# Performance work log

Measured on AMD Instinct MI355X. Metric: run time of the kernel, lower is better.

## Reference

```python
import jax, jax.numpy as jnp
import numpy as np

QMIN, QMAX = -128, 127  # 8-bit signed quantized range


def setup_inputs() -> dict:
    key = jax.random.key(0)
    k0, k1, k2, k3 = jax.random.split(key, 4)
    N, Cin, H, W = 64, 128, 56, 56
    Cout, K = 128, 3
    x = jax.random.randint(k0, (N, Cin, H, W), -128, 128, dtype=jnp.int32).astype(jnp.int8)
    weight = jax.random.randint(k1, (Cout, Cin, K, K), -128, 128, dtype=jnp.int32).astype(jnp.int8)
    # int32 bias (already shifted by -Zx*sum(W) in the original quantization flow)
    bias = jax.random.randint(k2, (Cout,), -4096, 4096, dtype=jnp.int32)
    input_scale = jnp.float32(0.02)
    weight_scale = jax.random.uniform(k3, (Cout,), minval=0.001, maxval=0.01, dtype=jnp.float32)  # per-channel
    output_scale = jnp.float32(0.05)
    input_zero_point = -3   # python int, constant
    output_zero_point = -2  # python int, constant
    return {"x": x, "weight": weight, "bias": bias,
            "input_scale": input_scale, "weight_scale": weight_scale,
            "output_scale": output_scale,
            "input_zero_point": input_zero_point,
            "output_zero_point": output_zero_point}


def reference(x, weight, bias, input_scale, weight_scale, output_scale,
              input_zero_point, output_zero_point):
    # pad spatial dims with the INPUT zero point (padding=(1,1), as in the torch module)
    xp = jnp.pad(x, ((0, 0), (0, 0), (1, 1), (1, 1)), constant_values=input_zero_point)
    acc = jax.lax.conv_general_dilated(
        xp.astype(jnp.int32), weight.astype(jnp.int32),
        window_strides=(1, 1), padding='VALID',
        rhs_dilation=(1, 1), dimension_numbers=('NCHW', 'OIHW', 'NCHW'))
    acc = acc + bias[None, :, None, None]                       # [N,Co,Ho,Wo] int32
    # requantize: per-output-channel scale, shift by output zero point
    scale = (input_scale * weight_scale / output_scale)[None, :, None, None]
    out = acc.astype(jnp.float32) * scale + jnp.float32(output_zero_point)
    return jnp.clip(jnp.round(out), QMIN, QMAX).astype(jnp.int8)
```

## Files before the change

kernel.cpp:

```cpp
#include <hip/hip_runtime.h>


#define CIN  128
#define COUT 128
#define HW   56
#define NPIX (HW * HW)
#define ROWS  4
#define QCOLS 58
#define XROW  (QCOLS * CIN)
#define XP_OFF 147456
#define XP_ROWS (64 * QCOLS)
#define STEPS 36

typedef int v4i  __attribute__((ext_vector_type(4)));
typedef int v16i __attribute__((ext_vector_type(16)));

__device__ __forceinline__ void gl16(const void* g, void* l) {
    __builtin_amdgcn_global_load_lds(
        (const __attribute__((address_space(1))) unsigned*)g,
        (__attribute__((address_space(3))) unsigned*)l, 16, 0, 0);
}

__global__ __launch_bounds__(256) void pack_w2(const int* __restrict__ w_g,
                                               unsigned* __restrict__ wp2) {
    int i = blockIdx.x * 256 + threadIdx.x;
    if (i >= 36 * 128 * 8) return;
    int dw   = i & 7;
    int cout = (i >> 3) & 127;
    int step = i >> 10;
    int t  = step >> 2;
    int cb = step & 3;
    unsigned d = 0;
#pragma unroll
    for (int b = 0; b < 4; ++b) {
        int ci = cb * 32 + dw * 4 + b;
        int v = w_g[(cout * CIN + ci) * 9 + t];
        d |= (unsigned)(v & 0xFF) << (8 * b);
    }
    int g  = (cout << 1) | (dw >> 2);
    int gs = g ^ ((g >> 3) & 7);
    wp2[step * 1024 + gs * 4 + (dw & 3)] = d;
}

#define LSTR 57
__global__ __launch_bounds__(256) void repack_x(const int* __restrict__ x_g,
                                                unsigned char* __restrict__ xp,
                                                const int* __restrict__ zp_in_p) {
    __shared__ int lx[CIN * LSTR];
    const int blk = blockIdx.x;
    const int n  = blk / QCOLS;
    const int hp = blk % QCOLS;
    const int tid = threadIdx.x;
    const unsigned zpd = (unsigned)((*zp_in_p) & 0xFF) * 0x01010101u;
    unsigned* row = (unsigned*)(xp + (size_t)blk * XROW);

    if (hp == 0 || hp == QCOLS - 1) {
#pragma unroll
        for (int it = 0; it < 8; ++it) {
            int d = it * 256 + tid;
            if (d < QCOLS * 32) row[d] = zpd;
        }
        return;
    }
    const int h = hp - 1;
    const int* xrow = x_g + (n * CIN * HW + h) * HW;
#pragma unroll
    for (int it = 0; it < 7; ++it) {
        int idx = it * 256 + tid;
        int ci  = idx / 14;
        int w4  = (idx - ci * 14) * 4;
        v4i L = *(const v4i*)(xrow + ci * NPIX + w4);
        int* ld = &lx[ci * LSTR + w4];
        ld[0] = L[0]; ld[1] = L[1]; ld[2] = L[2]; ld[3] = L[3];
    }
    __syncthreads();
#pragma unroll
    for (int it = 0; it < 8; ++it) {
        int d = it * 256 + tid;
        if (d < QCOLS * 32) {
            int wp  = d >> 5;
            int ci4 = d & 31;
            unsigned v = zpd;
            if (wp >= 1 && wp <= HW) {
                const int* lb = &lx[ci4 * 4 * LSTR + (wp - 1)];
                v = (unsigned)(lb[0] & 0xFF) |
                    ((unsigned)(lb[LSTR] & 0xFF) << 8) |
                    ((unsigned)(lb[2 * LSTR] & 0xFF) << 16) |
                    ((unsigned)(lb[3 * LSTR] & 0xFF) << 24);
            }
            row[d] = v;
        }
    }
}

__global__ __launch_bounds__(256, 2) void conv_mfma(
    const unsigned char* __restrict__ xp, const unsigned char* __restrict__ wp2b,
    const int* __restrict__ bias, const float* __restrict__ in_s,
    const float* __restrict__ w_s, const float* __restrict__ out_s,
    const int* __restrict__ zp_out_p, int* __restrict__ out) {
    __shared__ unsigned char xsb[45056];
    __shared__ float scs[COUT];
    __shared__ int   bis[COUT];

    const int n   = blockIdx.x / 14;
    const int ho0 = (blockIdx.x % 14) * ROWS;
    const int tid    = threadIdx.x;
    const int lane   = tid & 63;
    const int wave   = tid >> 6;
    const int lane31 = lane & 31;
    const int hi     = lane >> 5;
    const int hi4    = hi * 4;

    if (tid < COUT) {
        scs[tid] = ((*in_s) / (*out_s)) * w_s[tid];
        bis[tid] = bias[tid];
    }

    const unsigned char* win = xp + (size_t)(n * QCOLS + ho0) * XROW;
    const int qrel = lane >> 3;
    const int lof  = (qrel * 8 + ((lane & 7) ^ qrel)) * 16;
    for (int i = wave; i < 44; i += 4) {
        int off = i * 1024 + lof;
        if (i == 43 && qrel >= 4) off = 0;
        gl16(win + off, xsb + i * 1024);
    }
    __syncthreads();

    const unsigned* xs = (const unsigned*)xsb;
    int qb0, qb1;
    {
        int px0 = wave * 64 + lane31;
        int px1 = wave * 64 + 32 + lane31;
        if (px1 > ROWS * HW - 1) px1 = ROWS * HW - 1;
        qb0 = (px0 / HW) * QCOLS + (px0 % HW);
        qb1 = (px1 / HW) * QCOLS + (px1 % HW);
    }
    const unsigned char *bpA, *bpB, *bpC, *bpD;
    {
        int g0 = 0 * 64 + lane31 * 2 + hi;
        int g1 = 1 * 64 + lane31 * 2 + hi;
        int g2 = 2 * 64 + lane31 * 2 + hi;
        int g3 = 3 * 64 + lane31 * 2 + hi;
        bpA = wp2b + (g0 ^ ((g0 >> 3) & 7)) * 16;
        bpB = wp2b + (g1 ^ ((g1 >> 3) & 7)) * 16;
        bpC = wp2b + (g2 ^ ((g2 >> 3) & 7)) * 16;
        bpD = wp2b + (g3 ^ ((g3 >> 3) & 7)) * 16;
    }

    v16i acc[2][4];
#pragma unroll
    for (int i = 0; i < 2; ++i)
#pragma unroll
        for (int j = 0; j < 4; ++j) acc[i][j] = (v16i)0;

    v4i c0[4], c1[4], c2[4];
#define LOADB(DST, S)                                                        \
    {                                                                        \
        DST[0] = *(const v4i*)(bpA + (S) * 4096);                            \
        DST[1] = *(const v4i*)(bpB + (S) * 4096);                            \
        DST[2] = *(const v4i*)(bpC + (S) * 4096);                            \
        DST[3] = *(const v4i*)(bpD + (S) * 4096);                            \
    }
#define BODY(S, CUR, NX2)                                                    \
    {                                                                        \
        if ((S) + 2 < STEPS) LOADB(NX2, (S) + 2);                            \
        const int t2 = (S) >> 2, cb = (S) & 3;                               \
        const int kr = (t2 * 11) >> 5;                                       \
        const int dq = kr * QCOLS + (t2 - 3 * kr);                           \
        const int q0 = qb0 + dq, q1 = qb1 + dq;                              \
        v4i a0 = *(const v4i*)&xs[q0 * 32 + ((cb * 8 + hi4) ^ ((q0 & 7) << 2))]; \
        v4i a1 = *(const v4i*)&xs[q1 * 32 + ((cb * 8 + hi4) ^ ((q1 & 7) << 2))]; \
        acc[0][0] = __builtin_amdgcn_mfma_i32_32x32x32_i8(CUR[0], a0, acc[0][0], 0, 0, 0); \
        acc[0][1] = __builtin_amdgcn_mfma_i32_32x32x32_i8(CUR[1], a0, acc[0][1], 0, 0, 0); \
        acc[0][2] = __builtin_amdgcn_mfma_i32_32x32x32_i8(CUR[2], a0, acc[0][2], 0, 0, 0); \
        acc[0][3] = __builtin_amdgcn_mfma_i32_32x32x32_i8(CUR[3], a0, acc[0][3], 0, 0, 0); \
        acc[1][0] = __builtin_amdgcn_mfma_i32_32x32x32_i8(CUR[0], a1, acc[1][0], 0, 0, 0); \
        acc[1][1] = __builtin_amdgcn_mfma_i32_32x32x32_i8(CUR[1], a1, acc[1][1], 0, 0, 0); \
        acc[1][2] = __builtin_amdgcn_mfma_i32_32x32x32_i8(CUR[2], a1, acc[1][2], 0, 0, 0); \
        acc[1][3] = __builtin_amdgcn_mfma_i32_32x32x32_i8(CUR[3], a1, acc[1][3], 0, 0, 0); \
    }

    LOADB(c0, 0);
    LOADB(c1, 1);
#pragma unroll 1
    for (int uu = 0; uu < 12; ++uu) {
        const int s = uu * 3;
        BODY(s + 0, c0, c2);
        BODY(s + 1, c1, c0);
        BODY(s + 2, c2, c1);
    }
#undef BODY
#undef LOADB

    const float zpo = (float)(*zp_out_p);
#pragma unroll
    for (int i = 0; i < 2; ++i) {
        const int px = wave * 64 + i * 32 + lane31;
        if (px < ROWS * HW) {
            int* ob = out + n * COUT * NPIX + ho0 * HW + px;
#pragma unroll
            for (int nt = 0; nt < 4; ++nt) {
#pragma unroll
                for (int reg = 0; reg < 16; ++reg) {
                    int co = nt * 32 + (reg & 3) + 8 * (reg >> 2) + hi4;
                    float f = fmaf((float)(acc[i][nt][reg] + bis[co]), scs[co], zpo);
                    f = rintf(f);
                    f = fminf(fmaxf(f, -128.0f), 127.0f);
                    ob[co * NPIX] = (int)f;
                }
            }
        }
    }
}

extern "C" void kernel_launch(void* const* d_in, const int* in_sizes, int n_in,
                              void* d_out, int out_size, void* d_ws, size_t ws_size,
                              hipStream_t stream) {
    const int* x_g      = (const int*)d_in[0];
    const int* w_g      = (const int*)d_in[1];
    const int* bias     = (const int*)d_in[2];
    const float* in_s   = (const float*)d_in[3];
    const float* w_s    = (const float*)d_in[4];
    const float* out_s  = (const float*)d_in[5];
    const int* zp_in_p  = (const int*)d_in[6];
    const int* zp_out_p = (const int*)d_in[7];
    int* outp = (int*)d_out;
    unsigned* wp2 = (unsigned*)d_ws;
    unsigned char* xpp = (unsigned char*)d_ws + XP_OFF;

    pack_w2<<<(36 * 128 * 8 + 255) / 256, 256, 0, stream>>>(w_g, wp2);
    repack_x<<<XP_ROWS, 256, 0, stream>>>(x_g, xpp, zp_in_p);

    const int nblocks = 64 * (HW / ROWS);
    conv_mfma<<<nblocks, 256, 0, stream>>>(xpp, (const unsigned char*)wp2, bias,
                                           in_s, w_s, out_s, zp_out_p, outp);
}
```

Before: 86.74 us.

## Stage weight tiles through LDS with a 4-deep async global_load_lds pipeline

```diff
diff --git a/kernel.cpp b/kernel.cpp
--- a/kernel.cpp
+++ b/kernel.cpp
@@ -10,7 +10,6 @@
 #define XROW  (QCOLS * CIN)
 #define XP_OFF 147456
 #define XP_ROWS (64 * QCOLS)
-#define STEPS 36
 
 typedef int v4i  __attribute__((ext_vector_type(4)));
 typedef int v16i __attribute__((ext_vector_type(16)));
@@ -99,6 +98,7 @@
     const float* __restrict__ w_s, const float* __restrict__ out_s,
     const int* __restrict__ zp_out_p, int* __restrict__ out) {
     __shared__ unsigned char xsb[45056];
+    __shared__ unsigned char Bb[4][8192];
     __shared__ float scs[COUT];
     __shared__ int   bis[COUT];
 
@@ -116,6 +116,15 @@
         bis[tid] = bias[tid];
     }
 
+#define STAGEB(U)                                                             \
+    {                                                                         \
+        const unsigned char* bs = wp2b + (U) * 8192 + wave * 2048 + lane * 16;\
+        unsigned char* bd = &Bb[(U) & 3][wave * 2048];                        \
+        gl16(bs, bd);                                                         \
+        gl16(bs + 1024, bd + 1024);                                           \
+    }
+
+    STAGEB(0); STAGEB(1); STAGEB(2);
     const unsigned char* win = xp + (size_t)(n * QCOLS + ho0) * XROW;
     const int qrel = lane >> 3;
     const int lof  = (qrel * 8 + ((lane & 7) ^ qrel)) * 16;
@@ -135,16 +144,11 @@
         qb0 = (px0 / HW) * QCOLS + (px0 % HW);
         qb1 = (px1 / HW) * QCOLS + (px1 % HW);
     }
-    const unsigned char *bpA, *bpB, *bpC, *bpD;
-    {
-        int g0 = 0 * 64 + lane31 * 2 + hi;
-        int g1 = 1 * 64 + lane31 * 2 + hi;
-        int g2 = 2 * 64 + lane31 * 2 + hi;
-        int g3 = 3 * 64 + lane31 * 2 + hi;
-        bpA = wp2b + (g0 ^ ((g0 >> 3) & 7)) * 16;
-        bpB = wp2b + (g1 ^ ((g1 >> 3) & 7)) * 16;
-        bpC = wp2b + (g2 ^ ((g2 >> 3) & 7)) * 16;
-        bpD = wp2b + (g3 ^ ((g3 >> 3) & 7)) * 16;
+    int boff[4];
+#pragma unroll
+    for (int nt = 0; nt < 4; ++nt) {
+        int g = nt * 64 + lane31 * 2 + hi;
+        boff[nt] = (g ^ ((g >> 3) & 7)) * 16;
     }
 
     v16i acc[2][4];
@@ -153,44 +157,60 @@
 #pragma unroll
         for (int j = 0; j < 4; ++j) acc[i][j] = (v16i)0;
 
-    v4i c0[4], c1[4], c2[4];
-#define LOADB(DST, S)                                                        \
-    {                                                                        \
-        DST[0] = *(const v4i*)(bpA + (S) * 4096);                            \
-        DST[1] = *(const v4i*)(bpB + (S) * 4096);                            \
-        DST[2] = *(const v4i*)(bpC + (S) * 4096);                            \
-        DST[3] = *(const v4i*)(bpD + (S) * 4096);                            \
-    }
-#define BODY(S, CUR, NX2)                                                    \
-    {                                                                        \
-        if ((S) + 2 < STEPS) LOADB(NX2, (S) + 2);                            \
-        const int t2 = (S) >> 2, cb = (S) & 3;                               \
-        const int kr = (t2 * 11) >> 5;                                       \
-        const int dq = kr * QCOLS + (t2 - 3 * kr);                           \
-        const int q0 = qb0 + dq, q1 = qb1 + dq;                              \
-        v4i a0 = *(const v4i*)&xs[q0 * 32 + ((cb * 8 + hi4) ^ ((q0 & 7) << 2))]; \
-        v4i a1 = *(const v4i*)&xs[q1 * 32 + ((cb * 8 + hi4) ^ ((q1 & 7) << 2))]; \
-        acc[0][0] = __builtin_amdgcn_mfma_i32_32x32x32_i8(CUR[0], a0, acc[0][0], 0, 0, 0); \
-        acc[0][1] = __builtin_amdgcn_mfma_i32_32x32x32_i8(CUR[1], a0, acc[0][1], 0, 0, 0); \
-        acc[0][2] = __builtin_amdgcn_mfma_i32_32x32x32_i8(CUR[2], a0, acc[0][2], 0, 0, 0); \
-        acc[0][3] = __builtin_amdgcn_mfma_i32_32x32x32_i8(CUR[3], a0, acc[0][3], 0, 0, 0); \
-        acc[1][0] = __builtin_amdgcn_mfma_i32_32x32x32_i8(CUR[0], a1, acc[1][0], 0, 0, 0); \
-        acc[1][1] = __builtin_amdgcn_mfma_i32_32x32x32_i8(CUR[1], a1, acc[1][1], 0, 0, 0); \
-        acc[1][2] = __builtin_amdgcn_mfma_i32_32x32x32_i8(CUR[2], a1, acc[1][2], 0, 0, 0); \
-        acc[1][3] = __builtin_amdgcn_mfma_i32_32x32x32_i8(CUR[3], a1, acc[1][3], 0, 0, 0); \
-    }
-
-    LOADB(c0, 0);
-    LOADB(c1, 1);
+#define COMPUTE(U)                                                            \
+    {                                                                         \
+        const int t  = (U) >> 1;                                              \
+        const int kr = (t * 11) >> 5;                                         \
+        const int dq = kr * QCOLS + (t - 3 * kr);                             \
+        const int q0 = qb0 + dq, q1 = qb1 + dq;                               \
+        const int s0 = (q0 & 7) << 2, s1 = (q1 & 7) << 2;                     \
+        const unsigned char* bb = Bb[(U) & 3];                                \
+        __builtin_amdgcn_s_setprio(1);                                        \
+        _Pragma("unroll")                                                     \
+        for (int c = 0; c < 2; ++c) {                                         \
+            const int cb = ((U) & 1) * 2 + c;                                 \
+            v4i a0 = *(const v4i*)&xs[q0 * 32 + ((cb * 8 + hi4) ^ s0)];       \
+            v4i a1 = *(const v4i*)&xs[q1 * 32 + ((cb * 8 + hi4) ^ s1)];       \
+            const unsigned char* bc = bb + c * 4096;                          \
+            v4i b0 = *(const v4i*)(bc + boff[0]);                             \
+            v4i b1 = *(const v4i*)(bc + boff[1]);                             \
+            v4i b2 = *(const v4i*)(bc + boff[2]);                             \
+            v4i b3 = *(const v4i*)(bc + boff[3]);                             \
+            acc[0][0] = __builtin_amdgcn_mfma_i32_32x32x32_i8(b0, a0, acc[0][0], 0, 0, 0); \
+            acc[0][1] = __builtin_amdgcn_mfma_i32_32x32x32_i8(b1, a0, acc[0][1], 0, 0, 0); \
+            acc[0][2] = __builtin_amdgcn_mfma_i32_32x32x32_i8(b2, a0, acc[0][2], 0, 0, 0); \
+            acc[0][3] = __builtin_amdgcn_mfma_i32_32x32x32_i8(b3, a0, acc[0][3], 0, 0, 0); \
+            acc[1][0] = __builtin_amdgcn_mfma_i32_32x32x32_i8(b0, a1, acc[1][0], 0, 0, 0); \
+            acc[1][1] = __builtin_amdgcn_mfma_i32_32x32x32_i8(b1, a1, acc[1][1], 0, 0, 0); \
+            acc[1][2] = __builtin_amdgcn_mfma_i32_32x32x32_i8(b2, a1, acc[1][2], 0, 0, 0); \
+            acc[1][3] = __builtin_amdgcn_mfma_i32_32x32x32_i8(b3, a1, acc[1][3], 0, 0, 0); \
+        }                                                                     \
+        __builtin_amdgcn_s_setprio(0);                                        \
+    }
+
 #pragma unroll 1
-    for (int uu = 0; uu < 12; ++uu) {
-        const int s = uu * 3;
-        BODY(s + 0, c0, c2);
-        BODY(s + 1, c1, c0);
-        BODY(s + 2, c2, c1);
-    }
-#undef BODY
-#undef LOADB
+    for (int u = 0; u < 15; ++u) {
+        asm volatile("s_waitcnt vmcnt(4)" ::: "memory");
+        __builtin_amdgcn_sched_barrier(0);
+        __builtin_amdgcn_s_barrier();
+        asm volatile("" ::: "memory");
+        STAGEB(u + 3);
+        COMPUTE(u);
+    }
+    asm volatile("s_waitcnt vmcnt(4)" ::: "memory");
+    __builtin_amdgcn_sched_barrier(0);
+    __builtin_amdgcn_s_barrier();
+    COMPUTE(15);
+    asm volatile("s_waitcnt vmcnt(2)" ::: "memory");
+    __builtin_amdgcn_sched_barrier(0);
+    __builtin_amdgcn_s_barrier();
+    COMPUTE(16);
+    asm volatile("s_waitcnt vmcnt(0)" ::: "memory");
+    __builtin_amdgcn_sched_barrier(0);
+    __builtin_amdgcn_s_barrier();
+    COMPUTE(17);
+#undef COMPUTE
+#undef STAGEB
 
     const float zpo = (float)(*zp_out_p);
 #pragma unroll
```

After: 87.10 us. No clear change (+0.4%).

## Split work by output channels per wave and keep all weights in registers

Applied to the files above, without the earlier changes.

```diff
diff --git a/kernel.cpp b/kernel.cpp
--- a/kernel.cpp
+++ b/kernel.cpp
@@ -10,7 +10,6 @@
 #define XROW  (QCOLS * CIN)
 #define XP_OFF 147456
 #define XP_ROWS (64 * QCOLS)
-#define STEPS 36
 
 typedef int v4i  __attribute__((ext_vector_type(4)));
 typedef int v16i __attribute__((ext_vector_type(16)));
@@ -124,93 +123,89 @@
         if (i == 43 && qrel >= 4) off = 0;
         gl16(win + off, xsb + i * 1024);
     }
+
+    const int gg  = wave * 64 + lane31 * 2 + hi;
+    const int boff = (gg ^ ((gg >> 3) & 7)) * 16;
+    v4i breg[36];
+#pragma unroll
+    for (int s = 0; s < 36; ++s)
+        breg[s] = *(const v4i*)(wp2b + s * 4096 + boff);
+
     __syncthreads();
 
     const unsigned* xs = (const unsigned*)xsb;
-    int qb0, qb1;
+    const float zpo = (float)(*zp_out_p);
+
+#define ASTEP(ACC, QB, T, CB)                                                \
+    {                                                                        \
+        const int kr = ((T) * 11) >> 5;                                      \
+        const int dq = kr * QCOLS + ((T) - 3 * kr);                          \
+        const int q = (QB) + dq;                                             \
+        const int sx = (q & 7) << 2;                                         \
+        v4i a = *(const v4i*)&xs[q * 32 + (((CB) * 8 + hi4) ^ sx)];          \
+        ACC = __builtin_amdgcn_mfma_i32_32x32x32_i8(breg[(T) * 4 + (CB)], a, \
+                                                    ACC, 0, 0, 0);           \
+    }
+
+#define EPI(ACC, MT)                                                         \
+    {                                                                        \
+        const int px = (MT) * 32 + lane31;                                   \
+        int* ob = out + n * COUT * NPIX + ho0 * HW + px;                     \
+        _Pragma("unroll")                                                    \
+        for (int reg = 0; reg < 16; ++reg) {                                 \
+            const int co = wave * 32 + (reg & 3) + 8 * (reg >> 2) + hi4;     \
+            float f = fmaf((float)(ACC[reg] + bis[co]), scs[co], zpo);       \
+            f = rintf(f);                                                    \
+            f = fminf(fmaxf(f, -128.0f), 127.0f);                            \
+            ob[co * NPIX] = (int)f;                                          \
+        }                                                                    \
+    }
+
+#define PAIR(MT0, MT1)                                                       \
+    {                                                                        \
+        const int px0 = (MT0) * 32 + lane31;                                 \
+        const int px1 = (MT1) * 32 + lane31;                                 \
+        const int qb0 = (px0 / HW) * QCOLS + (px0 % HW);                     \
+        const int qb1 = (px1 / HW) * QCOLS + (px1 % HW);                     \
+        v16i acc0 = (v16i)0, acc1 = (v16i)0;                                 \
+        _Pragma("unroll")                                                    \
+        for (int t = 0; t < 9; ++t) {                                        \
+            _Pragma("unroll")                                                \
+            for (int cb = 0; cb < 4; ++cb) {                                 \
+                ASTEP(acc0, qb0, t, cb);                                     \
+                ASTEP(acc1, qb1, t, cb);                                     \
+            }                                                                \
+        }                                                                    \
+        EPI(acc0, MT0);                                                      \
+        EPI(acc1, MT1);                                                      \
+    }
+
+    PAIR(0, 1);
+    PAIR(2, 3);
+    PAIR(4, 5);
     {
-        int px0 = wave * 64 + lane31;
-        int px1 = wave * 64 + 32 + lane31;
-        if (px1 > ROWS * HW - 1) px1 = ROWS * HW - 1;
-        qb0 = (px0 / HW) * QCOLS + (px0 % HW);
-        qb1 = (px1 / HW) * QCOLS + (px1 % HW);
-    }
-    const unsigned char *bpA, *bpB, *bpC, *bpD;
-    {
-        int g0 = 0 * 64 + lane31 * 2 + hi;
-        int g1 = 1 * 64 + lane31 * 2 + hi;
-        int g2 = 2 * 64 + lane31 * 2 + hi;
-        int g3 = 3 * 64 + lane31 * 2 + hi;
-        bpA = wp2b + (g0 ^ ((g0 >> 3) & 7)) * 16;
-        bpB = wp2b + (g1 ^ ((g1 >> 3) & 7)) * 16;
-        bpC = wp2b + (g2 ^ ((g2 >> 3) & 7)) * 16;
-        bpD = wp2b + (g3 ^ ((g3 >> 3) & 7)) * 16;
-    }
-
-    v16i acc[2][4];
-#pragma unroll
-    for (int i = 0; i < 2; ++i)
-#pragma unroll
-        for (int j = 0; j < 4; ++j) acc[i][j] = (v16i)0;
-
-    v4i c0[4], c1[4], c2[4];
-#define LOADB(DST, S)                                                        \
-    {                                                                        \
-        DST[0] = *(const v4i*)(bpA + (S) * 4096);                            \
-        DST[1] = *(const v4i*)(bpB + (S) * 4096);                            \
-        DST[2] = *(const v4i*)(bpC + (S) * 4096);                            \
-        DST[3] = *(const v4i*)(bpD + (S) * 4096);                            \
-    }
-#define BODY(S, CUR, NX2)                                                    \
-    {                                                                        \
-        if ((S) + 2 < STEPS) LOADB(NX2, (S) + 2);                            \
-        const int t2 = (S) >> 2, cb = (S) & 3;                               \
-        const int kr = (t2 * 11) >> 5;                                       \
-        const int dq = kr * QCOLS + (t2 - 3 * kr);                           \
-        const int q0 = qb0 + dq, q1 = qb1 + dq;                              \
-        v4i a0 = *(const v4i*)&xs[q0 * 32 + ((cb * 8 + hi4) ^ ((q0 & 7) << 2))]; \
-        v4i a1 = *(const v4i*)&xs[q1 * 32 + ((cb * 8 + hi4) ^ ((q1 & 7) << 2))]; \
-        acc[0][0] = __builtin_amdgcn_mfma_i32_32x32x32_i8(CUR[0], a0, acc[0][0], 0, 0, 0); \
-        acc[0][1] = __builtin_amdgcn_mfma_i32_32x32x32_i8(CUR[1], a0, acc[0][1], 0, 0, 0); \
-        acc[0][2] = __builtin_amdgcn_mfma_i32_32x32x32_i8(CUR[2], a0, acc[0][2], 0, 0, 0); \
-        acc[0][3] = __builtin_amdgcn_mfma_i32_32x32x32_i8(CUR[3], a0, acc[0][3], 0, 0, 0); \
-        acc[1][0] = __builtin_amdgcn_mfma_i32_32x32x32_i8(CUR[0], a1, acc[1][0], 0, 0, 0); \
-        acc[1][1] = __builtin_amdgcn_mfma_i32_32x32x32_i8(CUR[1], a1, acc[1][1], 0, 0, 0); \
-        acc[1][2] = __builtin_amdgcn_mfma_i32_32x32x32_i8(CUR[2], a1, acc[1][2], 0, 0, 0); \
-        acc[1][3] = __builtin_amdgcn_mfma_i32_32x32x32_i8(CUR[3], a1, acc[1][3], 0, 0, 0); \
-    }
-
-    LOADB(c0, 0);
-    LOADB(c1, 1);
-#pragma unroll 1
-    for (int uu = 0; uu < 12; ++uu) {
-        const int s = uu * 3;
-        BODY(s + 0, c0, c2);
-        BODY(s + 1, c1, c0);
-        BODY(s + 2, c2, c1);
-    }
-#undef BODY
-#undef LOADB
-
-    const float zpo = (float)(*zp_out_p);
-#pragma unroll
-    for (int i = 0; i < 2; ++i) {
-        const int px = wave * 64 + i * 32 + lane31;
-        if (px < ROWS * HW) {
-            int* ob = out + n * COUT * NPIX + ho0 * HW + px;
-#pragma unroll
-            for (int nt = 0; nt < 4; ++nt) {
-#pragma unroll
-                for (int reg = 0; reg < 16; ++reg) {
-                    int co = nt * 32 + (reg & 3) + 8 * (reg >> 2) + hi4;
-                    float f = fmaf((float)(acc[i][nt][reg] + bis[co]), scs[co], zpo);
-                    f = rintf(f);
-                    f = fminf(fmaxf(f, -128.0f), 127.0f);
-                    ob[co * NPIX] = (int)f;
-                }
-            }
-        }
-    }
+        const int px0 = 6 * 32 + lane31;
+        const int qb0 = (px0 / HW) * QCOLS + (px0 % HW);
+        v16i acc0 = (v16i)0, acc1 = (v16i)0;
+#pragma unroll
+        for (int t = 0; t < 4; ++t)
+#pragma unroll
+            for (int cb = 0; cb < 4; ++cb) ASTEP(acc0, qb0, t, cb);
+        ASTEP(acc0, qb0, 4, 0);
+        ASTEP(acc0, qb0, 4, 1);
+        ASTEP(acc1, qb0, 4, 2);
+        ASTEP(acc1, qb0, 4, 3);
+#pragma unroll
+        for (int t = 5; t < 9; ++t)
+#pragma unroll
+            for (int cb = 0; cb < 4; ++cb) ASTEP(acc1, qb0, t, cb);
+#pragma unroll
+        for (int r = 0; r < 16; ++r) acc0[r] += acc1[r];
+        EPI(acc0, 6);
+    }
+#undef PAIR
+#undef EPI
+#undef ASTEP
 }
 
 extern "C" void kernel_launch(void* const* d_in, const int* in_sizes, int n_in,
```

Measured after the change: 95.47 us. +10.1%, slower.
